# Optimization experiments

Hardware: AMD Instinct MI355X
Metric: run time of the kernel (lower is better)

Reference implementation:

```python
import jax, jax.numpy as jnp
import numpy as np

NUM_HEADS = 12
TOP_K = 10


def setup_inputs() -> dict:
    key = jax.random.key(0)
    ks = jax.random.split(key, 6)
    B, LP, LS, D, V = 8, 64, 512, 768, 50257
    return {
        "prompt": jax.random.normal(ks[0], (B, LP, D), dtype=jnp.float32),
        "enc_emd": jax.random.normal(ks[1], (B, LS, D), dtype=jnp.float32),
        "word_emd": jax.random.normal(ks[2], (V, D), dtype=jnp.float32),
        "Wqkv": jax.random.normal(ks[3], (3 * D, D), dtype=jnp.float32) * (1.0 / np.sqrt(D)),
        "Wproj": jax.random.normal(ks[4], (D, D), dtype=jnp.float32) * (1.0 / np.sqrt(D)),
        "bproj": jnp.zeros((D,), dtype=jnp.float32),
    }


def reference(prompt, enc_emd, word_emd, Wqkv, Wproj, bproj):
    B, LP, D = prompt.shape
    LS = enc_emd.shape[1]
    H = NUM_HEADS
    hd = D // H
    scale = hd ** -0.5

    x = jnp.concatenate([prompt, enc_emd], axis=1)          # [B, L, D], L = LP+LS
    qkv = x @ Wqkv.T                                        # [B, L, 3D]
    qkv = qkv.reshape(B, LP + LS, 3, H, hd)
    q, k, v = (qkv[:, :, i].transpose(0, 2, 1, 3) for i in range(3))  # each [B, H, L, hd]

    attn = jnp.einsum("bhqd,bhkd->bhqk", q, k) * scale      # [B, H, L, L]
    attn = jax.nn.softmax(attn, axis=-1)
    out = jnp.einsum("bhqk,bhkd->bhqd", attn, v)            # [B, H, L, hd]
    out = out.transpose(0, 2, 1, 3).reshape(B, LP + LS, D)
    out = out @ Wproj.T + bproj                              # [B, L, D]

    # sim sums over the token axis l (einsum 'bld,vd->bv')
    sim = jnp.einsum("bld,vd->bv", out, word_emd)           # [B, V]
    _, topk_idx = jax.lax.top_k(sim, TOP_K)                 # [B, K]
    output = word_emd[topk_idx]                             # gather -> [B, K, D]
    return output
```

## Files before the change

kernel.cpp:

```cpp
#include <hip/hip_runtime.h>
#include <math.h>

#define B_ 8
#define LP_ 64
#define LS_ 512
#define L_ 576
#define D_ 768
#define H_ 12
#define HD_ 64
#define V_ 50257
#define TOPK_ 10
#define CHUNKS_ 64
#define CHUNK_SZ_ 786

#define M_QKV 4608
#define N_QKV 2304
#define K_QKV 768

typedef __attribute__((ext_vector_type(8))) short bhalf8;
typedef __attribute__((ext_vector_type(4))) float floatx4;

#define GLOAD16(gptr, lptr)                                              \
  __builtin_amdgcn_global_load_lds(                                      \
      (const __attribute__((address_space(1))) unsigned int*)(gptr),     \
      (__attribute__((address_space(3))) unsigned int*)(lptr), 16, 0, 0)

__device__ inline void bf16split(float f, unsigned short& h, unsigned short& lo) {
  unsigned int u = __float_as_uint(f);
  unsigned short hb = (unsigned short)((u + 0x7FFFu + ((u >> 16) & 1u)) >> 16);
  float hf = __uint_as_float(((unsigned int)hb) << 16);
  float lf = f - hf;
  unsigned int ul = __float_as_uint(lf);
  unsigned short lb = (unsigned short)((ul + 0x7FFFu + ((ul >> 16) & 1u)) >> 16);
  h = hb; lo = lb;
}

__global__ __launch_bounds__(256) void convert_split(
    const float* __restrict__ prompt, const float* __restrict__ enc,
    const float* __restrict__ Wqkv,
    unsigned short* __restrict__ Ahi, unsigned short* __restrict__ Alo,
    unsigned short* __restrict__ Bhi, unsigned short* __restrict__ Blo) {
  const int NA4 = M_QKV * K_QKV / 4;
  const int NB4 = N_QKV * K_QKV / 4;
  int i = blockIdx.x * 256 + threadIdx.x;
  if (i >= NA4 + NB4) return;
  const float* src;
  unsigned short *dh, *dl;
  int row, c4;
  if (i < NA4) {
    row = i / (K_QKV / 4);
    c4 = (i - row * (K_QKV / 4)) * 4;
    int b = row / L_, ll = row - (row / L_) * L_;
    src = (ll < LP_) ? (prompt + ((size_t)b * LP_ + ll) * D_ + c4)
                     : (enc + ((size_t)b * LS_ + (ll - LP_)) * D_ + c4);
    dh = Ahi + (size_t)row * K_QKV + c4;
    dl = Alo + (size_t)row * K_QKV + c4;
  } else {
    int j = i - NA4;
    row = j / (K_QKV / 4);
    c4 = (j - row * (K_QKV / 4)) * 4;
    src = Wqkv + (size_t)row * K_QKV + c4;
    dh = Bhi + (size_t)row * K_QKV + c4;
    dl = Blo + (size_t)row * K_QKV + c4;
  }
  float4 v = *(const float4*)src;
  ushort4 hv, lv;
  bf16split(v.x, hv.x, lv.x);
  bf16split(v.y, hv.y, lv.y);
  bf16split(v.z, hv.z, lv.z);
  bf16split(v.w, hv.w, lv.w);
  *(ushort4*)dh = hv;
  *(ushort4*)dl = lv;
}

__global__ __launch_bounds__(256) void qkv_mfma(
    const unsigned short* __restrict__ Ahi, const unsigned short* __restrict__ Alo,
    const unsigned short* __restrict__ Bhi, const unsigned short* __restrict__ Blo,
    unsigned short* __restrict__ Qhi, unsigned short* __restrict__ Qlo,
    unsigned short* __restrict__ Khi, unsigned short* __restrict__ Klo,
    float* __restrict__ Vv) {
  __shared__ unsigned short Ath[64 * 64];
  __shared__ unsigned short Atl[64 * 64];
  __shared__ unsigned short Bth[128 * 64];
  __shared__ unsigned short Btl[128 * 64];
  const int flat = blockIdx.x;
  const int swz = (flat & 7) * 162 + (flat >> 3);
  const int bx = swz % 18, by = swz / 18;
  const int n0 = bx * 128, m0 = by * 64;
  const int tid = threadIdx.x;
  const int l = tid & 63;
  const int w = tid >> 6;

  floatx4 acc[4][2];
#pragma unroll
  for (int i = 0; i < 4; ++i)
#pragma unroll
    for (int j = 0; j < 2; ++j) acc[i][j] = (floatx4){0.f, 0.f, 0.f, 0.f};

  const int r8 = l >> 3;
  const int cs = (l & 7) ^ r8;
  const int lm = l & 15;
  const int lk = l >> 4;

  for (int kt = 0; kt < 12; ++kt) {
    const int kk0 = kt * 64;
    __syncthreads();
#pragma unroll
    for (int i = 0; i < 2; ++i) {
      const int row = w * 16 + i * 8;
      const size_t ga = (size_t)(m0 + row + r8) * K_QKV + kk0 + cs * 8;
      GLOAD16(Ahi + ga, &Ath[row * 64]);
      GLOAD16(Alo + ga, &Atl[row * 64]);
    }
#pragma unroll
    for (int i = 0; i < 4; ++i) {
      const int row = w * 32 + i * 8;
      const size_t gb = (size_t)(n0 + row + r8) * K_QKV + kk0 + cs * 8;
      GLOAD16(Bhi + gb, &Bth[row * 64]);
      GLOAD16(Blo + gb, &Btl[row * 64]);
    }
    __syncthreads();

#pragma unroll
    for (int s = 0; s < 2; ++s) {
      bhalf8 ah[4], al[4], bh8[2], bl8[2];
#pragma unroll
      for (int f = 0; f < 4; ++f) {
        const int ma = f * 16 + lm;
        const int ca = (s * 4 + lk) ^ (ma & 7);
        ah[f] = *(const bhalf8*)&Ath[ma * 64 + ca * 8];
        al[f] = *(const bhalf8*)&Atl[ma * 64 + ca * 8];
      }
#pragma unroll
      for (int f = 0; f < 2; ++f) {
        const int nb = w * 32 + f * 16 + lm;
        const int cb2 = (s * 4 + lk) ^ (nb & 7);
        bh8[f] = *(const bhalf8*)&Bth[nb * 64 + cb2 * 8];
        bl8[f] = *(const bhalf8*)&Btl[nb * 64 + cb2 * 8];
      }
#pragma unroll
      for (int fm = 0; fm < 4; ++fm)
#pragma unroll
        for (int fn = 0; fn < 2; ++fn) {
          acc[fm][fn] = __builtin_amdgcn_mfma_f32_16x16x32_bf16(
              ah[fm], bh8[fn], acc[fm][fn], 0, 0, 0);
          acc[fm][fn] = __builtin_amdgcn_mfma_f32_16x16x32_bf16(
              al[fm], bh8[fn], acc[fm][fn], 0, 0, 0);
          acc[fm][fn] = __builtin_amdgcn_mfma_f32_16x16x32_bf16(
              ah[fm], bl8[fn], acc[fm][fn], 0, 0, 0);
        }
    }
  }

#pragma unroll
  for (int fm = 0; fm < 4; ++fm) {
#pragma unroll
    for (int fn = 0; fn < 2; ++fn) {
#pragma unroll
      for (int j = 0; j < 4; ++j) {
        int m = m0 + fm * 16 + lk * 4 + j;
        int n = n0 + w * 32 + fn * 16 + lm;
        int b = m / L_;
        int ll = m - b * L_;
        int part = n / D_;
        int rem = n - part * D_;
        int h = rem >> 6, e = rem & 63;
        size_t idx = (((size_t)b * H_ + h) * L_ + ll) * HD_ + e;
        float val = acc[fm][fn][j];
        if (part == 2) {
          Vv[idx] = val;
        } else {
          unsigned short hv, lv;
          bf16split(val, hv, lv);
          if (part == 0) { Qhi[idx] = hv; Qlo[idx] = lv; }
          else           { Khi[idx] = hv; Klo[idx] = lv; }
        }
      }
    }
  }
}

__global__ __launch_bounds__(256, 2) void attn_mfma(
    const unsigned short* __restrict__ Qhi, const unsigned short* __restrict__ Qlo,
    const unsigned short* __restrict__ Khi, const unsigned short* __restrict__ Klo,
    float* __restrict__ c) {
  __shared__ unsigned short Qh[64 * 64], Ql[64 * 64];
  __shared__ unsigned short Kh[192 * 64], Kl[192 * 64];
  __shared__ float c_lds[L_];
  const int qt = blockIdx.x;
  const int bh = blockIdx.y;
  const int tid = threadIdx.x;
  const int w = tid >> 6, l = tid & 63;
  const int lm = l & 15, lk = l >> 4;
  const int r8 = l >> 3;
  const int cs = (l & 7) ^ r8;

  for (int i = tid; i < L_; i += 256) c_lds[i] = 0.f;

  {
    const size_t gbase = ((size_t)bh * L_ + qt * 64) * HD_;
#pragma unroll
    for (int i = 0; i < 2; ++i) {
      int row = w * 16 + i * 8;
      GLOAD16(Qhi + gbase + (size_t)(row + r8) * HD_ + cs * 8, &Qh[row * 64]);
      GLOAD16(Qlo + gbase + (size_t)(row + r8) * HD_ + cs * 8, &Ql[row * 64]);
    }
  }

  floatx4 p[3][12];
#pragma unroll
  for (int kt = 0; kt < 3; ++kt)
#pragma unroll
    for (int fn = 0; fn < 12; ++fn) p[kt][fn] = (floatx4){0.f, 0.f, 0.f, 0.f};
  float zpart[4] = {0.f, 0.f, 0.f, 0.f};

#pragma unroll
  for (int kt = 0; kt < 3; ++kt) {
    __syncthreads();
    const size_t kb = ((size_t)bh * L_ + kt * 192) * HD_;
#pragma unroll
    for (int i = 0; i < 6; ++i) {
      int row = w * 48 + i * 8;
      GLOAD16(Khi + kb + (size_t)(row + r8) * HD_ + cs * 8, &Kh[row * 64]);
      GLOAD16(Klo + kb + (size_t)(row + r8) * HD_ + cs * 8, &Kl[row * 64]);
    }
    __syncthreads();
#pragma unroll
    for (int s = 0; s < 2; ++s) {
      const int ma = w * 16 + lm;
      const int ca = (s * 4 + lk) ^ (ma & 7);
      bhalf8 ah = *(const bhalf8*)&Qh[ma * 64 + ca * 8];
      bhalf8 al = *(const bhalf8*)&Ql[ma * 64 + ca * 8];
#pragma unroll
      for (int fn = 0; fn < 12; ++fn) {
        const int nb = fn * 16 + lm;
        const int cb2 = (s * 4 + lk) ^ (nb & 7);
        bhalf8 bh8 = *(const bhalf8*)&Kh[nb * 64 + cb2 * 8];
        bhalf8 bl8 = *(const bhalf8*)&Kl[nb * 64 + cb2 * 8];
        p[kt][fn] = __builtin_amdgcn_mfma_f32_16x16x32_bf16(ah, bh8, p[kt][fn], 0, 0, 0);
        p[kt][fn] = __builtin_amdgcn_mfma_f32_16x16x32_bf16(al, bh8, p[kt][fn], 0, 0, 0);
        p[kt][fn] = __builtin_amdgcn_mfma_f32_16x16x32_bf16(ah, bl8, p[kt][fn], 0, 0, 0);
      }
    }
#pragma unroll
    for (int fn = 0; fn < 12; ++fn)
#pragma unroll
      for (int j = 0; j < 4; ++j) {
        float e = __expf(p[kt][fn][j] * 0.125f);
        p[kt][fn][j] = e;
        zpart[j] += e;
      }
  }

  float invz[4];
#pragma unroll
  for (int j = 0; j < 4; ++j) {
    float z = zpart[j];
    z += __shfl_xor(z, 1);
    z += __shfl_xor(z, 2);
    z += __shfl_xor(z, 4);
    z += __shfl_xor(z, 8);
    invz[j] = 1.f / z;
  }

#pragma unroll
  for (int kt = 0; kt < 3; ++kt)
#pragma unroll
    for (int fn = 0; fn < 12; ++fn) {
      float cp = p[kt][fn][0] * invz[0] + p[kt][fn][1] * invz[1] +
                 p[kt][fn][2] * invz[2] + p[kt][fn][3] * invz[3];
      cp += __shfl_xor(cp, 16);
      cp += __shfl_xor(cp, 32);
      if (lk == 0) atomicAdd(&c_lds[kt * 192 + fn * 16 + lm], cp);
    }
  __syncthreads();
  for (int i = tid; i < L_; i += 256)
    atomicAdd(&c[(size_t)bh * L_ + i], c_lds[i]);
}

__global__ void cv_kernel(const float* __restrict__ c,
                          const float* __restrict__ Vv,
                          float* __restrict__ t) {
  const int bh = blockIdx.x;
  const int chunk = blockIdx.y;
  const int e = threadIdx.x;
  const float* cb = c + (size_t)bh * L_;
  const float* Vb = Vv + (size_t)bh * L_ * HD_;
  float acc = 0.f;
  const int k0 = chunk * 144;
  for (int k = k0; k < k0 + 144; ++k)
    acc = fmaf(cb[k], Vb[(size_t)k * HD_ + e], acc);
  int b = bh / H_, h = bh - (bh / H_) * H_;
  atomicAdd(&t[(size_t)b * D_ + h * HD_ + e], acc);
}

__global__ __launch_bounds__(256) void proj_kernel(
    const float* __restrict__ t, const float* __restrict__ Wp,
    const float* __restrict__ bp, float* __restrict__ s) {
  __shared__ float tl[B_ * D_];
  const int tid = threadIdx.x;
  for (int i = tid; i < (B_ * D_) / 4; i += 256)
    ((float4*)tl)[i] = ((const float4*)t)[i];
  __syncthreads();

  const int wv = tid >> 6, l = tid & 63;
  const int d = blockIdx.x * 4 + wv;
  const float* wrow = Wp + (size_t)d * D_;
  float acc[B_] = {};
#pragma unroll
  for (int k = 0; k < 3; ++k) {
    const int off = k * 256 + l * 4;
    float4 w4 = *(const float4*)(wrow + off);
#pragma unroll
    for (int b = 0; b < B_; ++b) {
      float4 t4 = *(const float4*)&tl[b * D_ + off];
      acc[b] = fmaf(w4.x, t4.x, acc[b]);
      acc[b] = fmaf(w4.y, t4.y, acc[b]);
      acc[b] = fmaf(w4.z, t4.z, acc[b]);
      acc[b] = fmaf(w4.w, t4.w, acc[b]);
    }
  }
#pragma unroll
  for (int off = 1; off < 64; off <<= 1)
#pragma unroll
    for (int b = 0; b < B_; ++b) acc[b] += __shfl_xor(acc[b], off);
  if (l == 0) {
    float bias = (float)L_ * bp[d];
#pragma unroll
    for (int b = 0; b < B_; ++b) s[(size_t)b * D_ + d] = acc[b] + bias;
  }
}

#define SIM_COMPUTE(K, CWA, CWB)                                            \
  {                                                                         \
    const float* sbp = &s2[((K) * 16 + p) * 36];                            \
    float4 sj[8];                                                           \
    _Pragma("unroll")                                                       \
    for (int jj = 0; jj < 8; ++jj) sj[jj] = *(const float4*)(sbp + jj * 4); \
    float ca4[4] = {CWA.x, CWA.y, CWA.z, CWA.w};                            \
    float cb4[4] = {CWB.x, CWB.y, CWB.z, CWB.w};                            \
    _Pragma("unroll")                                                       \
    for (int j = 0; j < 4; ++j) {                                           \
      accA[0] = fmaf(ca4[j], sj[2 * j].x, accA[0]);                         \
      accA[1] = fmaf(ca4[j], sj[2 * j].y, accA[1]);                         \
      accA[2] = fmaf(ca4[j], sj[2 * j].z, accA[2]);                         \
      accA[3] = fmaf(ca4[j], sj[2 * j].w, accA[3]);                         \
      accA[4] = fmaf(ca4[j], sj[2 * j + 1].x, accA[4]);                     \
      accA[5] = fmaf(ca4[j], sj[2 * j + 1].y, accA[5]);                     \
      accA[6] = fmaf(ca4[j], sj[2 * j + 1].z, accA[6]);                     \
      accA[7] = fmaf(ca4[j], sj[2 * j + 1].w, accA[7]);                     \
      accB[0] = fmaf(cb4[j], sj[2 * j].x, accB[0]);                         \
      accB[1] = fmaf(cb4[j], sj[2 * j].y, accB[1]);                         \
      accB[2] = fmaf(cb4[j], sj[2 * j].z, accB[2]);                         \
      accB[3] = fmaf(cb4[j], sj[2 * j].w, accB[3]);                         \
      accB[4] = fmaf(cb4[j], sj[2 * j + 1].x, accB[4]);                     \
      accB[5] = fmaf(cb4[j], sj[2 * j + 1].y, accB[5]);                     \
      accB[6] = fmaf(cb4[j], sj[2 * j + 1].z, accB[6]);                     \
      accB[7] = fmaf(cb4[j], sj[2 * j + 1].w, accB[7]);                     \
    }                                                                       \
  }

#define SIM_STEP(K, SA, SB)                                                 \
  {                                                                         \
    float4 cwa = SA, cwb = SB;                                              \
    if ((K) + 4 < 12) {                                                     \
      SA = *(const float4*)(wpA + ((K) + 4) * 64);                          \
      SB = *(const float4*)(wpB + ((K) + 4) * 64);                          \
    }                                                                       \
    SIM_COMPUTE(K, cwa, cwb)                                                \
  }

__global__ __launch_bounds__(256) void sim_kernel(
    const float* __restrict__ s, const float* __restrict__ w,
    float* __restrict__ sim) {
  __shared__ float s2[192 * 36];
  const int tid = threadIdx.x;
  for (int e = tid; e < 6144; e += 256) {
    int b = e / 768;
    int d = e - b * 768;
    int k = d >> 6, pj = d & 63;
    int p = pj >> 2, j = pj & 3;
    s2[(k * 16 + p) * 36 + j * 8 + b] = s[e];
  }
  __syncthreads();

  const int wv = tid >> 6, l = tid & 63;
  const int g = l >> 4, p = l & 15;
  const int base = blockIdx.x * 32 + wv * 8;
  const int rA = base + g, rB = base + g + 4;
  const int cA = (rA < V_) ? rA : (V_ - 1);
  const int cB = (rB < V_) ? rB : (V_ - 1);
  const float* wpA = w + (size_t)cA * D_ + p * 4;
  const float* wpB = w + (size_t)cB * D_ + p * 4;

  float accA[8] = {}, accB[8] = {};
  float4 A0 = *(const float4*)(wpA);
  float4 B0 = *(const float4*)(wpB);
  float4 A1 = *(const float4*)(wpA + 64);
  float4 B1 = *(const float4*)(wpB + 64);
  float4 A2 = *(const float4*)(wpA + 128);
  float4 B2 = *(const float4*)(wpB + 128);
  float4 A3 = *(const float4*)(wpA + 192);
  float4 B3 = *(const float4*)(wpB + 192);

  SIM_STEP(0, A0, B0)
  SIM_STEP(1, A1, B1)
  SIM_STEP(2, A2, B2)
  SIM_STEP(3, A3, B3)
  SIM_STEP(4, A0, B0)
  SIM_STEP(5, A1, B1)
  SIM_STEP(6, A2, B2)
  SIM_STEP(7, A3, B3)
  SIM_STEP(8, A0, B0)
  SIM_STEP(9, A1, B1)
  SIM_STEP(10, A2, B2)
  SIM_STEP(11, A3, B3)

#pragma unroll
  for (int off = 1; off < 16; off <<= 1) {
#pragma unroll
    for (int b = 0; b < 8; ++b) {
      accA[b] += __shfl_xor(accA[b], off);
      accB[b] += __shfl_xor(accB[b], off);
    }
  }
  if (p == 0) {
#pragma unroll
    for (int b = 0; b < 8; ++b) {
      if (rA < V_) sim[(size_t)b * V_ + rA] = accA[b];
      if (rB < V_) sim[(size_t)b * V_ + rB] = accB[b];
    }
  }
}

__global__ __launch_bounds__(256) void topk_stage1(
    const float* __restrict__ sim, float* __restrict__ cv,
    int* __restrict__ ci) {
  __shared__ float vals[CHUNK_SZ_];
  __shared__ float bv[256];
  __shared__ int bi[256];
  const int chunk = blockIdx.x, b = blockIdx.y, tid = threadIdx.x;
  const int base = chunk * CHUNK_SZ_;
  const float* row = sim + (size_t)b * V_;
  for (int i = tid; i < CHUNK_SZ_; i += 256) {
    int v = base + i;
    vals[i] = (v < V_) ? row[v] : -INFINITY;
  }
  __syncthreads();
  for (int k = 0; k < TOPK_; ++k) {
    float best = -INFINITY;
    int besti = CHUNK_SZ_;
    for (int i = tid; i < CHUNK_SZ_; i += 256) {
      float x = vals[i];
      if (x > best) { best = x; besti = i; }
    }
    bv[tid] = best; bi[tid] = besti;
    __syncthreads();
    for (int off = 128; off > 0; off >>= 1) {
      if (tid < off) {
        float ov = bv[tid + off]; int oi = bi[tid + off];
        if (ov > bv[tid] || (ov == bv[tid] && oi < bi[tid])) {
          bv[tid] = ov; bi[tid] = oi;
        }
      }
      __syncthreads();
    }
    if (tid == 0) {
      int slot = (b * CHUNKS_ + chunk) * TOPK_ + k;
      cv[slot] = bv[0];
      ci[slot] = base + bi[0];
      if (bi[0] < CHUNK_SZ_) vals[bi[0]] = -INFINITY;
    }
    __syncthreads();
  }
}

__global__ __launch_bounds__(256) void topk_stage2(
    const float* __restrict__ cv, const int* __restrict__ ci,
    int* __restrict__ topk) {
  const int NC = CHUNKS_ * TOPK_;
  __shared__ float vals[CHUNKS_ * TOPK_];
  __shared__ int gidx[CHUNKS_ * TOPK_];
  __shared__ float bv[256];
  __shared__ int bi[256];
  const int b = blockIdx.x, tid = threadIdx.x;
  for (int i = tid; i < NC; i += 256) {
    vals[i] = cv[(size_t)b * NC + i];
    gidx[i] = ci[(size_t)b * NC + i];
  }
  __syncthreads();
  for (int k = 0; k < TOPK_; ++k) {
    float best = -INFINITY;
    int bslot = NC;
    for (int i = tid; i < NC; i += 256) {
      float x = vals[i];
      if (x > best) { best = x; bslot = i; }
    }
    bv[tid] = best; bi[tid] = bslot;
    __syncthreads();
    for (int off = 128; off > 0; off >>= 1) {
      if (tid < off) {
        float ov = bv[tid + off]; int oi = bi[tid + off];
        if (ov > bv[tid] || (ov == bv[tid] && oi < bi[tid])) {
          bv[tid] = ov; bi[tid] = oi;
        }
      }
      __syncthreads();
    }
    if (tid == 0) {
      int slot = bi[0];
      topk[b * TOPK_ + k] = (slot < NC) ? gidx[slot] : 0;
      if (slot < NC) vals[slot] = -INFINITY;
    }
    __syncthreads();
  }
}

__global__ void gather_kernel(const int* __restrict__ topk,
                              const float* __restrict__ w,
                              float* __restrict__ out) {
  const int bk = blockIdx.x;
  const int idx = topk[bk];
  const int t4 = threadIdx.x << 2;
  *(float4*)(out + (size_t)bk * D_ + t4) =
      *(const float4*)(w + (size_t)idx * D_ + t4);
}

extern "C" void kernel_launch(void* const* d_in, const int* in_sizes, int n_in,
                              void* d_out, int out_size, void* d_ws,
                              size_t ws_size, hipStream_t stream) {
  const float* prompt = (const float*)d_in[0];
  const float* enc    = (const float*)d_in[1];
  const float* wemd   = (const float*)d_in[2];
  const float* Wqkv   = (const float*)d_in[3];
  const float* Wproj  = (const float*)d_in[4];
  const float* bproj  = (const float*)d_in[5];
  float* out = (float*)d_out;

  float* ws = (float*)d_ws;
  const size_t QSZ = (size_t)B_ * H_ * L_ * HD_;
  float* Vv   = ws;
  float* c    = Vv + QSZ;
  float* t    = c + (size_t)B_ * H_ * L_;
  float* s    = t + (size_t)B_ * D_;
  float* sim  = s + (size_t)B_ * D_;
  float* cand_v = sim + (size_t)B_ * V_;
  int* cand_i   = (int*)(cand_v + (size_t)B_ * CHUNKS_ * TOPK_);
  int* topk     = cand_i + (size_t)B_ * CHUNKS_ * TOPK_;
  unsigned short* Qhi = (unsigned short*)(topk + B_ * TOPK_ + 64);
  unsigned short* Qlo = Qhi + QSZ;
  unsigned short* Khi = Qlo + QSZ;
  unsigned short* Klo = Khi + QSZ;
  unsigned short* Ahi = Klo + QSZ;
  unsigned short* Alo = Ahi + (size_t)M_QKV * K_QKV;
  unsigned short* Bhi = Alo + (size_t)M_QKV * K_QKV;
  unsigned short* Blo = Bhi + (size_t)N_QKV * K_QKV;

  hipMemsetAsync(c, 0, ((size_t)B_ * H_ * L_ + (size_t)B_ * D_) * sizeof(float),
                 stream);

  const int NCONV = (M_QKV * K_QKV + N_QKV * K_QKV) / 4;
  convert_split<<<(NCONV + 255) / 256, 256, 0, stream>>>(
      prompt, enc, Wqkv, Ahi, Alo, Bhi, Blo);
  qkv_mfma<<<(M_QKV / 64) * (N_QKV / 128), 256, 0, stream>>>(
      Ahi, Alo, Bhi, Blo, Qhi, Qlo, Khi, Klo, Vv);
  attn_mfma<<<dim3(9, 96), 256, 0, stream>>>(Qhi, Qlo, Khi, Klo, c);
  cv_kernel<<<dim3(96, 4), 64, 0, stream>>>(c, Vv, t);
  proj_kernel<<<D_ / 4, 256, 0, stream>>>(t, Wproj, bproj, s);
  sim_kernel<<<(V_ + 31) / 32, 256, 0, stream>>>(s, wemd, sim);
  topk_stage1<<<dim3(CHUNKS_, B_), 256, 0, stream>>>(sim, cand_v, cand_i);
  topk_stage2<<<B_, 256, 0, stream>>>(cand_v, cand_i, topk);
  gather_kernel<<<80, 192, 0, stream>>>(topk, wemd, out);
}
```

Before: 201.2 us.

## Double-buffer QKV GEMM LDS tiles with K-step 32 and async prefetch

The QKV split-bf16 GEMM now uses two LDS buffers with K tiles of 32 instead of one buffer with K tiles of 64. The next tile is loaded through global_load_lds while MFMAs run on the current one, with explicit vmcnt waits and barriers in place of the two __syncthreads per iteration. The goal is to hide global-to-LDS latency behind compute. In exchange there are twice as many iterations, each with two barriers, and a new XOR swizzle that has to stay correct for a 32-wide row.

```diff
diff --git a/kernel.cpp b/kernel.cpp
--- a/kernel.cpp
+++ b/kernel.cpp
@@ -79,10 +79,10 @@
     unsigned short* __restrict__ Qhi, unsigned short* __restrict__ Qlo,
     unsigned short* __restrict__ Khi, unsigned short* __restrict__ Klo,
     float* __restrict__ Vv) {
-  __shared__ unsigned short Ath[64 * 64];
-  __shared__ unsigned short Atl[64 * 64];
-  __shared__ unsigned short Bth[128 * 64];
-  __shared__ unsigned short Btl[128 * 64];
+  __shared__ unsigned short Ath[2][64 * 32];
+  __shared__ unsigned short Atl[2][64 * 32];
+  __shared__ unsigned short Bth[2][128 * 32];
+  __shared__ unsigned short Btl[2][128 * 32];
   const int flat = blockIdx.x;
   const int swz = (flat & 7) * 162 + (flat >> 3);
   const int bx = swz % 18, by = swz / 18;
@@ -97,60 +97,74 @@
 #pragma unroll
     for (int j = 0; j < 2; ++j) acc[i][j] = (floatx4){0.f, 0.f, 0.f, 0.f};
 
-  const int r8 = l >> 3;
-  const int cs = (l & 7) ^ r8;
+  const int r4 = l >> 2;
+  const int cs = (l & 3) ^ ((l >> 3) & 3);
   const int lm = l & 15;
   const int lk = l >> 4;
-
-  for (int kt = 0; kt < 12; ++kt) {
-    const int kk0 = kt * 64;
-    __syncthreads();
-#pragma unroll
-    for (int i = 0; i < 2; ++i) {
-      const int row = w * 16 + i * 8;
-      const size_t ga = (size_t)(m0 + row + r8) * K_QKV + kk0 + cs * 8;
-      GLOAD16(Ahi + ga, &Ath[row * 64]);
-      GLOAD16(Alo + ga, &Atl[row * 64]);
-    }
-#pragma unroll
-    for (int i = 0; i < 4; ++i) {
-      const int row = w * 32 + i * 8;
-      const size_t gb = (size_t)(n0 + row + r8) * K_QKV + kk0 + cs * 8;
-      GLOAD16(Bhi + gb, &Bth[row * 64]);
-      GLOAD16(Blo + gb, &Btl[row * 64]);
-    }
-    __syncthreads();
-
-#pragma unroll
-    for (int s = 0; s < 2; ++s) {
-      bhalf8 ah[4], al[4], bh8[2], bl8[2];
-#pragma unroll
-      for (int f = 0; f < 4; ++f) {
-        const int ma = f * 16 + lm;
-        const int ca = (s * 4 + lk) ^ (ma & 7);
-        ah[f] = *(const bhalf8*)&Ath[ma * 64 + ca * 8];
-        al[f] = *(const bhalf8*)&Atl[ma * 64 + ca * 8];
+  const int cb = lk ^ ((lm >> 1) & 3);
+
+#define QKV_STAGE(kt_, buf_)                                                  \
+  {                                                                           \
+    const int kk0_ = (kt_) * 32;                                              \
+    {                                                                         \
+      const int rowA_ = w * 16;                                               \
+      const size_t ga_ = (size_t)(m0 + rowA_ + r4) * K_QKV + kk0_ + cs * 8;   \
+      GLOAD16(Ahi + ga_, &Ath[buf_][rowA_ * 32]);                             \
+      GLOAD16(Alo + ga_, &Atl[buf_][rowA_ * 32]);                             \
+    }                                                                         \
+    _Pragma("unroll")                                                         \
+    for (int i_ = 0; i_ < 2; ++i_) {                                          \
+      const int rowB_ = w * 32 + i_ * 16;                                     \
+      const size_t gb_ = (size_t)(n0 + rowB_ + r4) * K_QKV + kk0_ + cs * 8;   \
+      GLOAD16(Bhi + gb_, &Bth[buf_][rowB_ * 32]);                             \
+      GLOAD16(Blo + gb_, &Btl[buf_][rowB_ * 32]);                             \
+    }                                                                         \
+  }
+
+  QKV_STAGE(0, 0);
+  int cur = 0;
+  for (int kt = 0; kt < 24; ++kt) {
+    if (kt + 1 < 24) {
+      QKV_STAGE(kt + 1, cur ^ 1);
+      __builtin_amdgcn_sched_barrier(0);
+      asm volatile("s_waitcnt vmcnt(6)" ::: "memory");
+    } else {
+      asm volatile("s_waitcnt vmcnt(0)" ::: "memory");
+    }
+    __builtin_amdgcn_sched_barrier(0);
+    __builtin_amdgcn_s_barrier();
+
+    bhalf8 ah[4], al[4], bh8[2], bl8[2];
+#pragma unroll
+    for (int f = 0; f < 4; ++f) {
+      const int ma = f * 16 + lm;
+      const int oa = ma * 32 + cb * 8;
+      ah[f] = *(const bhalf8*)&Ath[cur][oa];
+      al[f] = *(const bhalf8*)&Atl[cur][oa];
+    }
+#pragma unroll
+    for (int f = 0; f < 2; ++f) {
+      const int nb = w * 32 + f * 16 + lm;
+      const int ob = nb * 32 + cb * 8;
+      bh8[f] = *(const bhalf8*)&Bth[cur][ob];
+      bl8[f] = *(const bhalf8*)&Btl[cur][ob];
+    }
+#pragma unroll
+    for (int fm = 0; fm < 4; ++fm)
+#pragma unroll
+      for (int fn = 0; fn < 2; ++fn) {
+        acc[fm][fn] = __builtin_amdgcn_mfma_f32_16x16x32_bf16(
+            ah[fm], bh8[fn], acc[fm][fn], 0, 0, 0);
+        acc[fm][fn] = __builtin_amdgcn_mfma_f32_16x16x32_bf16(
+            al[fm], bh8[fn], acc[fm][fn], 0, 0, 0);
+        acc[fm][fn] = __builtin_amdgcn_mfma_f32_16x16x32_bf16(
+            ah[fm], bl8[fn], acc[fm][fn], 0, 0, 0);
       }
-#pragma unroll
-      for (int f = 0; f < 2; ++f) {
-        const int nb = w * 32 + f * 16 + lm;
-        const int cb2 = (s * 4 + lk) ^ (nb & 7);
-        bh8[f] = *(const bhalf8*)&Bth[nb * 64 + cb2 * 8];
-        bl8[f] = *(const bhalf8*)&Btl[nb * 64 + cb2 * 8];
-      }
-#pragma unroll
-      for (int fm = 0; fm < 4; ++fm)
-#pragma unroll
-        for (int fn = 0; fn < 2; ++fn) {
-          acc[fm][fn] = __builtin_amdgcn_mfma_f32_16x16x32_bf16(
-              ah[fm], bh8[fn], acc[fm][fn], 0, 0, 0);
-          acc[fm][fn] = __builtin_amdgcn_mfma_f32_16x16x32_bf16(
-              al[fm], bh8[fn], acc[fm][fn], 0, 0, 0);
-          acc[fm][fn] = __builtin_amdgcn_mfma_f32_16x16x32_bf16(
-              ah[fm], bl8[fn], acc[fm][fn], 0, 0, 0);
-        }
-    }
-  }
+    __builtin_amdgcn_sched_barrier(0);
+    __builtin_amdgcn_s_barrier();
+    cur ^= 1;
+  }
+#undef QKV_STAGE
 
 #pragma unroll
   for (int fm = 0; fm < 4; ++fm) {
```

Result: slower. 223.1 us (+10.9%).
